# Optimization experiments

Hardware: AMD Instinct MI355X
Metric: run time of the kernel (lower is better)

## Reference

```python
import jax, jax.numpy as jnp
import numpy as np

NUM_IN, NUM_OUT, K, G = 128, 128, 3, 5
SIZE = NUM_IN * NUM_OUT
BATCH = 512


def _extend_grid(grid, k):
    # pykan-style extension: add k uniformly spaced knots on each side
    h = (grid[:, -1:] - grid[:, :1]) / (grid.shape[1] - 1)
    for _ in range(k):
        grid = jnp.concatenate([grid[:, :1] - h, grid, grid[:, -1:] + h], axis=1)
    return grid


def _b_batch(x, grid, k):
    # Cox-de Boor recursion. x: (size, batch), grid: (size, G+1)
    g = _extend_grid(grid, k)[:, :, None]          # (size, G+1+2k, 1)
    xe = x[:, None, :]                             # (size, 1, batch)
    B = ((xe >= g[:, :-1]) & (xe < g[:, 1:])).astype(x.dtype)  # degree-0: (size, G+2k, batch)
    for p in range(1, k + 1):
        B = (xe - g[:, :-(p + 1)]) / (g[:, p:-1] - g[:, :-(p + 1)]) * B[:, :-1] \
          + (g[:, p + 1:] - xe) / (g[:, p + 1:] - g[:, 1:-p]) * B[:, 1:]
    return B                                       # (size, G+k, batch)


def _coef_to_curve(x_eval, grid, coef, k):
    return jnp.einsum('sj,sjb->sb', coef, _b_batch(x_eval, grid, k))


def setup_inputs():
    key = jax.random.key(0)
    k1, k2 = jax.random.split(key)
    x = jax.random.normal(k1, (BATCH, NUM_IN), dtype=jnp.float32)
    knots = jnp.tile(jnp.linspace(-1.0, 1.0, G + 1, dtype=jnp.float32)[None, :], (SIZE, 1))
    coef = jax.random.normal(k2, (SIZE, G + K), dtype=jnp.float32) * 0.1
    scale_b = jnp.ones((SIZE, 1), dtype=jnp.float32)
    scale_spline = jnp.ones((SIZE, 1), dtype=jnp.float32)
    mask = jnp.ones((SIZE,), dtype=jnp.float32)
    return {"x": x, "scale_b": scale_b, "scale_spline": scale_spline,
            "coef": coef, "mask": mask, "knots": knots}


def reference(x, scale_b, scale_spline, coef, mask, knots):
    batch = x.shape[0]
    # x.unsqueeze(1).repeat(1, num_out, 1).reshape(-1, size).T -> (size, batch)
    pre_acts = jnp.broadcast_to(x[:, None, :], (batch, NUM_OUT, NUM_IN)).reshape(batch, SIZE).T
    post_splines = _coef_to_curve(pre_acts, knots, coef, K) * mask[:, None]
    post_acts = scale_b * jax.nn.silu(pre_acts) + scale_spline * post_splines
    # reshape(num_in, num_out, batch).permute(2,0,1).sum(dim=1) as in the original
    y = post_acts.reshape(NUM_IN, NUM_OUT, batch).transpose(2, 0, 1).sum(axis=1)
    return (y, pre_acts.T, post_splines.T, post_acts.T)
```

## Files before the change

### kernel.cpp

```cpp
#include <hip/hip_runtime.h>
#include <math.h>


#define N_IN   128
#define SIZEK  16384
#define BATCH  512

#define TB 4
#define CO 4

__global__ __launch_bounds__(256) void kan_fwd(
    const float* __restrict__ x,
    const float* __restrict__ scale_b,
    const float* __restrict__ scale_spline,
    const float* __restrict__ coef,
    const float* __restrict__ mask,
    const float* __restrict__ knots,
    float* __restrict__ y,
    float* __restrict__ pre_out,
    float* __restrict__ spl_out,
    float* __restrict__ post_out)
{
    const int g  = blockIdx.x * blockDim.x + threadIdx.x;
    const int i  = g & 127;
    const int r  = g >> 7;
    const int oc = r & 31;
    const int bg = r >> 5;
    const int o0 = oc << 2;
    const int b0 = bg << 2;

    float xv[TB], sil[TB], ysum[TB];
#pragma unroll
    for (int t = 0; t < TB; ++t) {
        const float xx = x[(b0 + t) * N_IN + i];
        xv[t]   = xx;
        sil[t]  = xx / (1.0f + __expf(-xx));
        ysum[t] = 0.0f;
    }

    float e0v[CO], ihv[CO], mkv[CO], sbv[CO], ssv[CO];
    float4 cA[CO], cB[CO];
#pragma unroll
    for (int oo = 0; oo < CO; ++oo) {
        const int s = ((o0 + oo) << 7) | i;
        const float k0 = knots[s * 6];
        const float k5 = knots[s * 6 + 5];
        const float h  = (k5 - k0) * 0.2f;
        ihv[oo] = 1.0f / h;
        e0v[oo] = k0 - 3.0f * h;
        mkv[oo] = mask[s];
        sbv[oo] = scale_b[s];
        ssv[oo] = scale_spline[s];
        const float4* c4 = (const float4*)(coef + (size_t)s * 8);
        cA[oo] = c4[0];
        cB[oo] = c4[1];
    }

    const bool same_lane =
        (e0v[1] == e0v[0]) && (ihv[1] == ihv[0]) &&
        (e0v[2] == e0v[0]) && (ihv[2] == ihv[0]) &&
        (e0v[3] == e0v[0]) && (ihv[3] == ihv[0]);

    if (__all(same_lane)) {
        const float e0   = e0v[0];
        const float invh = ihv[0];
#pragma unroll
        for (int t = 0; t < TB; ++t) {
            const float u  = (xv[t] - e0) * invh;
            const float mf = floorf(u);
            const int   m  = (int)mf;
            const float tt = u - mf;
            const bool inr = (m >= 0) && (m <= 10);

            const float t2  = tt * tt;
            const float t3  = t2 * tt;
            const float omt = 1.0f - tt;
            float w[4];
            w[0] = omt * omt * omt * (1.0f / 6.0f);
            w[1] = (3.0f * t3 - 6.0f * t2 + 4.0f) * (1.0f / 6.0f);
            w[2] = (-3.0f * t3 + 3.0f * t2 + 3.0f * tt + 1.0f) * (1.0f / 6.0f);
            w[3] = t3 * (1.0f / 6.0f);

            const int jlo = m - 3;
            int   jc[4];
            float wv[4];
#pragma unroll
            for (int rr = 0; rr < 4; ++rr) {
                const int j = jlo + rr;
                jc[rr] = min(max(j, 0), 7);
                wv[rr] = (inr && j >= 0 && j <= 7) ? w[rr] : 0.0f;
            }

#pragma unroll
            for (int oo = 0; oo < CO; ++oo) {
                const int s = ((o0 + oo) << 7) | i;
                const float c0 = cA[oo].x, c1 = cA[oo].y, c2 = cA[oo].z, c3 = cA[oo].w;
                const float c4 = cB[oo].x, c5 = cB[oo].y, c6 = cB[oo].z, c7 = cB[oo].w;

                float spline = 0.0f;
#pragma unroll
                for (int rr = 0; rr < 4; ++rr) {
                    const int jcr = jc[rr];
                    const float s01   = (jcr & 1) ? c1 : c0;
                    const float s23   = (jcr & 1) ? c3 : c2;
                    const float s45   = (jcr & 1) ? c5 : c4;
                    const float s67   = (jcr & 1) ? c7 : c6;
                    const float s0123 = (jcr & 2) ? s23 : s01;
                    const float s4567 = (jcr & 2) ? s67 : s45;
                    const float c     = (jcr & 4) ? s4567 : s0123;
                    spline = fmaf(c, wv[rr], spline);
                }

                const float splm = spline * mkv[oo];
                const float post = fmaf(sbv[oo], sil[t], ssv[oo] * splm);

                const size_t idx = (size_t)(b0 + t) * SIZEK + (size_t)s;
                pre_out[idx]  = xv[t];
                spl_out[idx]  = splm;
                post_out[idx] = post;
                ysum[t] += post;
            }
        }
    } else {
#pragma unroll
        for (int oo = 0; oo < CO; ++oo) {
            const int s = ((o0 + oo) << 7) | i;
            const float e0   = e0v[oo];
            const float invh = ihv[oo];
            const float mk   = mkv[oo];
            const float sb   = sbv[oo];
            const float ss   = ssv[oo];
            const float c0 = cA[oo].x, c1 = cA[oo].y, c2 = cA[oo].z, c3 = cA[oo].w;
            const float c4 = cB[oo].x, c5 = cB[oo].y, c6 = cB[oo].z, c7 = cB[oo].w;

#pragma unroll
            for (int t = 0; t < TB; ++t) {
                const float u  = (xv[t] - e0) * invh;
                const float mf = floorf(u);
                const int   m  = (int)mf;
                const float tt = u - mf;
                const bool inr = (m >= 0) && (m <= 10);

                const float t2  = tt * tt;
                const float t3  = t2 * tt;
                const float omt = 1.0f - tt;
                float w[4];
                w[0] = omt * omt * omt * (1.0f / 6.0f);
                w[1] = (3.0f * t3 - 6.0f * t2 + 4.0f) * (1.0f / 6.0f);
                w[2] = (-3.0f * t3 + 3.0f * t2 + 3.0f * tt + 1.0f) * (1.0f / 6.0f);
                w[3] = t3 * (1.0f / 6.0f);

                const int jlo = m - 3;
                float spline = 0.0f;
#pragma unroll
                for (int rr = 0; rr < 4; ++rr) {
                    const int j  = jlo + rr;
                    const int jcr = min(max(j, 0), 7);
                    const float s01   = (jcr & 1) ? c1 : c0;
                    const float s23   = (jcr & 1) ? c3 : c2;
                    const float s45   = (jcr & 1) ? c5 : c4;
                    const float s67   = (jcr & 1) ? c7 : c6;
                    const float s0123 = (jcr & 2) ? s23 : s01;
                    const float s4567 = (jcr & 2) ? s67 : s45;
                    const float c     = (jcr & 4) ? s4567 : s0123;
                    const float wvv = (inr && j >= 0 && j <= 7) ? w[rr] : 0.0f;
                    spline = fmaf(c, wvv, spline);
                }

                const float splm = spline * mk;
                const float post = fmaf(sb, sil[t], ss * splm);

                const size_t idx = (size_t)(b0 + t) * SIZEK + (size_t)s;
                pre_out[idx]  = xv[t];
                spl_out[idx]  = splm;
                post_out[idx] = post;
                ysum[t] += post;
            }
        }
    }

#pragma unroll
    for (int t = 0; t < TB; ++t)
        atomicAdd(&y[(b0 + t) * N_IN + i], ysum[t]);
}

extern "C" void kernel_launch(void* const* d_in, const int* in_sizes, int n_in,
                              void* d_out, int out_size, void* d_ws, size_t ws_size,
                              hipStream_t stream) {
    const float* x            = (const float*)d_in[0];
    const float* scale_b      = (const float*)d_in[1];
    const float* scale_spline = (const float*)d_in[2];
    const float* coef         = (const float*)d_in[3];
    const float* mask         = (const float*)d_in[4];
    const float* knots        = (const float*)d_in[5];

    float* out  = (float*)d_out;
    float* y    = out;
    float* pre  = y + 512 * 128;
    float* spl  = pre + (size_t)512 * 16384;
    float* post = spl + (size_t)512 * 16384;

    (void)hipMemsetAsync(y, 0, 512 * 128 * sizeof(float), stream);

    dim3 grid(2048), block(256);
    kan_fwd<<<grid, block, 0, stream>>>(x, scale_b, scale_spline, coef, mask,
                                        knots, y, pre, spl, post);
}
```

Baseline: 121.6 us.

## Stage spline coefficients in LDS and index them instead of select trees

Each block now cooperatively loads the coefficients for its four output columns into padded shared memory. Spline evaluation indexes those coefficients directly instead of running a seven-select tree per basis term. The thread-to-work mapping is also swapped so that a block covers a fixed output group across batch groups, which makes the shared tile valid for every thread in the block. This trades register-held coefficients and selects for LDS reads plus a barrier, and it changes the store access pattern across blocks.

```diff
diff --git a/kernel.cpp b/kernel.cpp
--- a/kernel.cpp
+++ b/kernel.cpp
@@ -8,6 +8,7 @@
 
 #define TB 4
 #define CO 4
+#define CPAD 9
 
 __global__ __launch_bounds__(256) void kan_fwd(
     const float* __restrict__ x,
@@ -21,13 +22,30 @@
     float* __restrict__ spl_out,
     float* __restrict__ post_out)
 {
-    const int g  = blockIdx.x * blockDim.x + threadIdx.x;
+    __shared__ float shc[512 * CPAD];
+
+    const int tid = threadIdx.x;
+    const int g  = blockIdx.x * 256 + tid;
     const int i  = g & 127;
     const int r  = g >> 7;
-    const int oc = r & 31;
-    const int bg = r >> 5;
+    const int oc = r >> 7;
+    const int bg = r & 127;
     const int o0 = oc << 2;
     const int b0 = bg << 2;
+    const int s_base = o0 << 7;
+
+    {
+        const float4* src = (const float4*)(coef + (size_t)s_base * 8);
+#pragma unroll
+        for (int k = 0; k < 4; ++k) {
+            const int f4  = k * 256 + tid;
+            const float4 v = src[f4];
+            const int row = f4 >> 1;
+            const int col = (f4 & 1) << 2;
+            float* d = &shc[row * CPAD + col];
+            d[0] = v.x; d[1] = v.y; d[2] = v.z; d[3] = v.w;
+        }
+    }
 
     float xv[TB], sil[TB], ysum[TB];
 #pragma unroll
@@ -39,7 +57,6 @@
     }
 
     float e0v[CO], ihv[CO], mkv[CO], sbv[CO], ssv[CO];
-    float4 cA[CO], cB[CO];
 #pragma unroll
     for (int oo = 0; oo < CO; ++oo) {
         const int s = ((o0 + oo) << 7) | i;
@@ -51,10 +68,9 @@
         mkv[oo] = mask[s];
         sbv[oo] = scale_b[s];
         ssv[oo] = scale_spline[s];
-        const float4* c4 = (const float4*)(coef + (size_t)s * 8);
-        cA[oo] = c4[0];
-        cB[oo] = c4[1];
-    }
+    }
+
+    __syncthreads();
 
     const bool same_lane =
         (e0v[1] == e0v[0]) && (ihv[1] == ihv[0]) &&
@@ -94,22 +110,12 @@
 #pragma unroll
             for (int oo = 0; oo < CO; ++oo) {
                 const int s = ((o0 + oo) << 7) | i;
-                const float c0 = cA[oo].x, c1 = cA[oo].y, c2 = cA[oo].z, c3 = cA[oo].w;
-                const float c4 = cB[oo].x, c5 = cB[oo].y, c6 = cB[oo].z, c7 = cB[oo].w;
+                const float* __restrict__ cs = &shc[(oo * 128 + i) * CPAD];
 
                 float spline = 0.0f;
 #pragma unroll
-                for (int rr = 0; rr < 4; ++rr) {
-                    const int jcr = jc[rr];
-                    const float s01   = (jcr & 1) ? c1 : c0;
-                    const float s23   = (jcr & 1) ? c3 : c2;
-                    const float s45   = (jcr & 1) ? c5 : c4;
-                    const float s67   = (jcr & 1) ? c7 : c6;
-                    const float s0123 = (jcr & 2) ? s23 : s01;
-                    const float s4567 = (jcr & 2) ? s67 : s45;
-                    const float c     = (jcr & 4) ? s4567 : s0123;
-                    spline = fmaf(c, wv[rr], spline);
-                }
+                for (int rr = 0; rr < 4; ++rr)
+                    spline = fmaf(cs[jc[rr]], wv[rr], spline);
 
                 const float splm = spline * mkv[oo];
                 const float post = fmaf(sbv[oo], sil[t], ssv[oo] * splm);
@@ -130,8 +136,7 @@
             const float mk   = mkv[oo];
             const float sb   = sbv[oo];
             const float ss   = ssv[oo];
-            const float c0 = cA[oo].x, c1 = cA[oo].y, c2 = cA[oo].z, c3 = cA[oo].w;
-            const float c4 = cB[oo].x, c5 = cB[oo].y, c6 = cB[oo].z, c7 = cB[oo].w;
+            const float* __restrict__ cs = &shc[(oo * 128 + i) * CPAD];
 
 #pragma unroll
             for (int t = 0; t < TB; ++t) {
@@ -154,17 +159,10 @@
                 float spline = 0.0f;
 #pragma unroll
                 for (int rr = 0; rr < 4; ++rr) {
-                    const int j  = jlo + rr;
+                    const int j   = jlo + rr;
                     const int jcr = min(max(j, 0), 7);
-                    const float s01   = (jcr & 1) ? c1 : c0;
-                    const float s23   = (jcr & 1) ? c3 : c2;
-                    const float s45   = (jcr & 1) ? c5 : c4;
-                    const float s67   = (jcr & 1) ? c7 : c6;
-                    const float s0123 = (jcr & 2) ? s23 : s01;
-                    const float s4567 = (jcr & 2) ? s67 : s45;
-                    const float c     = (jcr & 4) ? s4567 : s0123;
                     const float wvv = (inr && j >= 0 && j <= 7) ? w[rr] : 0.0f;
-                    spline = fmaf(c, wvv, spline);
+                    spline = fmaf(cs[jcr], wvv, spline);
                 }
 
                 const float splm = spline * mk;
```

After: 121.2 us. No clear change (-0.3%).
